# Performance work log

Measured on AMD Instinct MI355X. Metric: run time of the kernel, lower is better.

Reference implementation:

```python
import jax, jax.numpy as jnp
import numpy as np

N = 4096
IN_F = 256
OUT_F = 64
HEADS = 8
ALPHA = 0.2  # LeakyReLU negative slope


def setup_inputs() -> dict:
    key = jax.random.key(0)
    k1, k2, k3, k4 = jax.random.split(key, 4)
    X = jax.random.normal(k1, (N, IN_F), dtype=jnp.float32)
    adj = jax.random.randint(k2, (N, N), 0, 2, dtype=jnp.int32)
    # self-loops so every row has at least one neighbor (softmax well-defined)
    idx = jnp.arange(N)
    adj = adj.at[idx, idx].set(1)
    W = jax.random.normal(k3, (HEADS, IN_F, OUT_F), dtype=jnp.float32) * 0.05
    a = jax.random.normal(k4, (HEADS, 2 * OUT_F, 1), dtype=jnp.float32) * 0.05
    return {"X": X, "adj": adj, "W": W, "a": a}


def reference(X, adj, W, a):
    # H: [heads, N, F]
    H = jnp.einsum('ni,hio->hno', X, W)
    F_ = H.shape[-1]
    # cat([h_i, h_j]) @ a  ==  h_i @ a[:F] + h_j @ a[F:]
    a1 = a[:, :F_, 0]   # [heads, F]
    a2 = a[:, F_:, 0]   # [heads, F]
    f1 = jnp.einsum('hnf,hf->hn', H, a1)  # score contribution of row node i
    f2 = jnp.einsum('hnf,hf->hn', H, a2)  # score contribution of col node j
    e = jax.nn.leaky_relu(f1[:, :, None] + f2[:, None, :], negative_slope=ALPHA)  # [heads, N, N]
    e = jnp.where(adj[None, :, :] == 0, -jnp.inf, e)
    attention = jax.nn.softmax(e, axis=-1)
    # dropout omitted (eval mode)
    H_out = jnp.einsum('hnm,hmf->hnf', attention, H)  # [heads, N, F]
    return H_out.mean(axis=0)  # [N, F]
```

## Files before the change

kernel.cpp:

```cpp
#include <hip/hip_runtime.h>
#include <hip/hip_bf16.h>

#define N_NODES 4096
#define IN_F 256
#define OUT_F 64
#define HEADS 8
#define ALPHA 0.2f

typedef _Float16 f16x8 __attribute__((ext_vector_type(8)));
typedef float f32x4 __attribute__((ext_vector_type(4)));
union U4 { uint4 u; f16x8 h; unsigned w[4]; };

#define WFRAG_OFF 0
#define BFRAG_OFF (WFRAG_OFF + 8*8*4*64*8*2)
#define F1_OFF    (BFRAG_OFF + 8*128*4*64*8*2)
#define GP_OFF    (F1_OFF + 8*4096*4)
#define GN_OFF    (GP_OFF + 8*4096*2)
#define ADJ_OFF   (GN_OFF + 8*4096*2)

static __device__ __forceinline__ unsigned pkmul(unsigned a, unsigned b) {
  unsigned r; asm("v_pk_mul_f16 %0, %1, %2" : "=v"(r) : "v"(a), "v"(b)); return r;
}
static __device__ __forceinline__ unsigned pkmax(unsigned a, unsigned b) {
  unsigned r; asm("v_pk_max_f16 %0, %1, %2" : "=v"(r) : "v"(a), "v"(b)); return r;
}
static __device__ __forceinline__ unsigned short f2h_bits(float f) {
  return __builtin_bit_cast(unsigned short, (_Float16)f);
}

__global__ __launch_bounds__(256) void k_misc(
    const int* __restrict__ adj, const float* __restrict__ W,
    unsigned long long* __restrict__ bits, _Float16* __restrict__ wfrag,
    float* __restrict__ out) {
  int b = blockIdx.x, t = threadIdx.x;
  if (b < 2048) {
    int lane = t & 63;
    int waveid = b * 4 + (t >> 6);
    for (int it = 0; it < 32; ++it) {
      int widx = waveid + it * 8192;
      int v = adj[(size_t)widx * 64 + lane];
      unsigned long long m = __ballot(v != 0);
      if (lane == 0) bits[widx] = m;
    }
  } else {
    int h = b - 2048;
    for (int pos = t; pos < 2048; pos += 256) {
      int kt = pos >> 8, ct = (pos >> 6) & 3, l = pos & 63;
      int lr = l & 15, lg = l >> 4;
#pragma unroll
      for (int e = 0; e < 8; ++e)
        wfrag[(size_t)(((h*8 + kt)*4 + ct)*64 + l) * 8 + e]
          = (_Float16)W[(size_t)(h*256 + kt*32 + lg*8 + e) * 64 + ct*16 + lr];
    }
    float4* oz = ((float4*)out) + h * 8192;
    float4 zz = make_float4(0.f, 0.f, 0.f, 0.f);
    for (int q = t; q < 8192; q += 256) oz[q] = zz;
  }
}

__global__ __launch_bounds__(256) void k_hf(
    const float* __restrict__ X, const _Float16* __restrict__ wfrag,
    const float* __restrict__ a, _Float16* __restrict__ bfrag,
    float* __restrict__ f1, _Float16* __restrict__ Gp, _Float16* __restrict__ Gn) {
  int b = blockIdx.x, t = threadIdx.x;
  int h = b & 7, rb = b >> 3;
  int w = t >> 6, l = t & 63;
  int i0 = rb * 64 + w * 16;
  int r = l & 15, g = l >> 4;
  const U4* wv = (const U4*)wfrag;
  f32x4 z = {0.f, 0.f, 0.f, 0.f};
  f32x4 acc[4] = {z, z, z, z};
#pragma unroll
  for (int kt = 0; kt < 8; ++kt) {
    const float4* xr = (const float4*)(X + (size_t)(i0 + r) * 256 + (kt*4 + g) * 8);
    float4 x0 = xr[0], x1 = xr[1];
    U4 af;
    af.h[0] = (_Float16)x0.x; af.h[1] = (_Float16)x0.y;
    af.h[2] = (_Float16)x0.z; af.h[3] = (_Float16)x0.w;
    af.h[4] = (_Float16)x1.x; af.h[5] = (_Float16)x1.y;
    af.h[6] = (_Float16)x1.z; af.h[7] = (_Float16)x1.w;
#pragma unroll
    for (int ct = 0; ct < 4; ++ct) {
      U4 bv = wv[((h*8 + kt)*4 + ct)*64 + l];
      acc[ct] = __builtin_amdgcn_mfma_f32_16x16x32_f16(af.h, bv.h, acc[ct], 0, 0, 0);
    }
  }
  int jb = i0 + g*4;
#pragma unroll
  for (int ct = 0; ct < 4; ++ct) {
    size_t base = ((((size_t)h*128 + (jb>>5))*4 + ct)*64 + ((jb>>3)&3)*16 + r) * 8
                  + (jb & 7);
    union { short4 s; _Float16 hh[4]; } sv;
#pragma unroll
    for (int ri = 0; ri < 4; ++ri) sv.hh[ri] = (_Float16)acc[ct][ri];
    *(short4*)(bfrag + base) = sv.s;
  }
  float a1v[4], a2v[4];
#pragma unroll
  for (int ct = 0; ct < 4; ++ct) {
    a1v[ct] = a[h*128 + ct*16 + r];
    a2v[ct] = a[h*128 + 64 + ct*16 + r];
  }
#pragma unroll
  for (int ri = 0; ri < 4; ++ri) {
    float s1 = acc[0][ri]*a1v[0] + acc[1][ri]*a1v[1]
             + acc[2][ri]*a1v[2] + acc[3][ri]*a1v[3];
    float s2 = acc[0][ri]*a2v[0] + acc[1][ri]*a2v[1]
             + acc[2][ri]*a2v[2] + acc[3][ri]*a2v[3];
#pragma unroll
    for (int off = 1; off < 16; off <<= 1) {
      s1 += __shfl_xor(s1, off);
      s2 += __shfl_xor(s2, off);
    }
    if (r == 0) {
      int row = i0 + g*4 + ri;
      f1[h*4096 + row] = s1;
      Gp[h*4096 + row] = (_Float16)__expf(s2);
      Gn[h*4096 + row] = (_Float16)__expf(ALPHA * s2);
    }
  }
}

#define ATTN_BODY(PF, JT, DOPF) {                                              \
  U4 gp, gn;                                                                   \
  gp.u = Gs[0][(JT)*4 + g].u;                                                  \
  gn.u = Gs[1][(JT)*4 + g].u;                                                  \
  U4 b0, b1, b2, b3;                                                           \
  b0.u = PF[0]; b1.u = PF[1]; b2.u = PF[2]; b3.u = PF[3];                      \
  _Pragma("unroll")                                                            \
  for (int rg = 0; rg < 4; ++rg) {                                             \
    unsigned wm = Lb[rg*16 + r][JT];                                           \
    U4 av;                                                                     \
    _Pragma("unroll")                                                          \
    for (int p = 0; p < 4; ++p) {                                              \
      unsigned pm = pkmax(pkmul(Epp[rg], gp.w[p]), pkmul(Enn[rg], gn.w[p]));   \
      av.w[p] = pm & MLUT[(wm >> (g8 + 2*p)) & 3u];                            \
    }                                                                          \
    acc[rg][0] = __builtin_amdgcn_mfma_f32_16x16x32_f16(av.h, b0.h, acc[rg][0], 0,0,0); \
    acc[rg][1] = __builtin_amdgcn_mfma_f32_16x16x32_f16(av.h, b1.h, acc[rg][1], 0,0,0); \
    acc[rg][2] = __builtin_amdgcn_mfma_f32_16x16x32_f16(av.h, b2.h, acc[rg][2], 0,0,0); \
    acc[rg][3] = __builtin_amdgcn_mfma_f32_16x16x32_f16(av.h, b3.h, acc[rg][3], 0,0,0); \
    dn[rg]     = __builtin_amdgcn_mfma_f32_16x16x32_f16(av.h, bones.h, dn[rg], 0,0,0);  \
  }                                                                            \
  if (DOPF) {                                                                  \
    _Pragma("unroll")                                                          \
    for (int c = 0; c < 4; ++c) PF[c] = bfh[((JT) + 2)*256 + c*64];            \
  }                                                                            \
}

#define WRBUF(buf) {                                                           \
  _Pragma("unroll")                                                            \
  for (int rg = 0; rg < 4; ++rg) {                                             \
    _Pragma("unroll")                                                          \
    for (int ct = 0; ct < 4; ++ct) buf[rg*4 + ct][l] = acc[rg][ct];            \
    buf[16 + rg][l] = dn[rg];                                                  \
  } }
#define ADBUF(buf) {                                                           \
  _Pragma("unroll")                                                            \
  for (int rg = 0; rg < 4; ++rg) {                                             \
    _Pragma("unroll")                                                          \
    for (int ct = 0; ct < 4; ++ct) acc[rg][ct] += buf[rg*4 + ct][l];           \
    dn[rg] += buf[16 + rg][l];                                                 \
  } }

__global__ __launch_bounds__(512) void k_attn(
    const float* __restrict__ f1, const unsigned int* __restrict__ adjbits,
    const _Float16* __restrict__ Gp, const _Float16* __restrict__ Gn,
    const _Float16* __restrict__ bfrag, float* __restrict__ out) {
  __shared__ __align__(16) char smem[49408];
  __shared__ unsigned MLUT[4];
  unsigned (*Lb)[129] = (unsigned(*)[129])smem;
  U4 (*Gs)[512] = (U4(*)[512])(smem + 33024);
  f32x4 (*red0)[64] = (f32x4(*)[64])smem;
  f32x4 (*red1)[64] = (f32x4(*)[64])(smem + 20480);
  int b = blockIdx.x;
  int h = b & 7, rs = b >> 3;
  int i0 = rs * 64;
  int t = threadIdx.x, jq = t >> 6, l = t & 63;
  int r = l & 15, g = l >> 4, g8 = g * 8;
  if (t < 4) MLUT[t] = ((t & 1) ? 0xFFFFu : 0u) | ((t & 2) ? 0xFFFF0000u : 0u);
  for (int q = t; q < 8192; q += 512)
    Lb[q >> 7][q & 127] = adjbits[(size_t)(i0 + (q >> 7)) * 128 + (q & 127)];
  Gs[0][t].u = ((const uint4*)(Gp + (size_t)h * 4096))[t];
  Gs[1][t].u = ((const uint4*)(Gn + (size_t)h * 4096))[t];
  unsigned Epp[4], Enn[4];
#pragma unroll
  for (int rg = 0; rg < 4; ++rg) {
    float f1r = f1[h * N_NODES + i0 + rg*16 + r];
    unsigned short ep = f2h_bits(__expf(f1r));
    unsigned short en = f2h_bits(__expf(ALPHA * f1r));
    Epp[rg] = ep | ((unsigned)ep << 16);
    Enn[rg] = en | ((unsigned)en << 16);
  }
  unsigned ov = (r == 0) ? 0x3C003C00u : 0u;
  U4 bones; bones.u = make_uint4(ov, ov, ov, ov);
  const uint4* bfh = (const uint4*)bfrag + (size_t)h * 32768 + l;
  int jt0 = jq * 16;
  uint4 pA[4], pB[4];
#pragma unroll
  for (int c = 0; c < 4; ++c) pA[c] = bfh[jt0 * 256 + c*64];
#pragma unroll
  for (int c = 0; c < 4; ++c) pB[c] = bfh[(jt0 + 1) * 256 + c*64];
  __syncthreads();
  f32x4 z = {0.f,0.f,0.f,0.f};
  f32x4 acc[4][4] = {{z,z,z,z},{z,z,z,z},{z,z,z,z},{z,z,z,z}};
  f32x4 dn[4] = {z,z,z,z};
  for (int q2 = 0; q2 < 8; ++q2) {
    ATTN_BODY(pA, jt0 + q2*2,     (q2 < 7));
    ATTN_BODY(pB, jt0 + q2*2 + 1, (q2 < 7));
  }
  __syncthreads();
  if (jq == 1) WRBUF(red0);
  if (jq == 5) WRBUF(red1);
  __syncthreads();
  if (jq == 0) ADBUF(red0);
  if (jq == 4) ADBUF(red1);
  __syncthreads();
  if (jq == 3) WRBUF(red0);
  if (jq == 7) WRBUF(red1);
  __syncthreads();
  if (jq == 2) ADBUF(red0);
  if (jq == 6) ADBUF(red1);
  __syncthreads();
  if (jq == 2) WRBUF(red0);
  if (jq == 6) WRBUF(red1);
  __syncthreads();
  if (jq == 0) ADBUF(red0);
  if (jq == 4) ADBUF(red1);
  __syncthreads();
  if (jq == 4) WRBUF(red0);
  __syncthreads();
  if (jq == 0) {
    ADBUF(red0);
#pragma unroll
    for (int rg = 0; rg < 4; ++rg)
#pragma unroll
      for (int ri = 0; ri < 4; ++ri) {
        float den = __shfl(dn[rg][ri], l & 48);
        float sc = 0.125f / den;
        float* op = out + (size_t)(i0 + rg*16 + g*4 + ri) * 64;
        atomicAdd(op + r,      acc[rg][0][ri] * sc);
        atomicAdd(op + 16 + r, acc[rg][1][ri] * sc);
        atomicAdd(op + 32 + r, acc[rg][2][ri] * sc);
        atomicAdd(op + 48 + r, acc[rg][3][ri] * sc);
      }
  }
}

extern "C" void kernel_launch(void* const* d_in, const int* in_sizes, int n_in,
                              void* d_out, int out_size, void* d_ws, size_t ws_size,
                              hipStream_t stream) {
  const float* X = (const float*)d_in[0];
  const int* adj = (const int*)d_in[1];
  const float* W = (const float*)d_in[2];
  const float* a = (const float*)d_in[3];
  float* out = (float*)d_out;
  char* ws = (char*)d_ws;

  _Float16* wfrag = (_Float16*)(ws + WFRAG_OFF);
  _Float16* bfrag = (_Float16*)(ws + BFRAG_OFF);
  float* f1 = (float*)(ws + F1_OFF);
  _Float16* Gp = (_Float16*)(ws + GP_OFF);
  _Float16* Gn = (_Float16*)(ws + GN_OFF);
  unsigned long long* bits64 = (unsigned long long*)(ws + ADJ_OFF);
  const unsigned int* bits32 = (const unsigned int*)(ws + ADJ_OFF);

  k_misc<<<dim3(2056), dim3(256), 0, stream>>>(adj, W, bits64, wfrag, out);
  k_hf<<<dim3(512), dim3(256), 0, stream>>>(X, wfrag, a, bfrag, f1, Gp, Gn);
  k_attn<<<dim3(512), dim3(512), 0, stream>>>(f1, bits32, Gp, Gn, bfrag, out);
}
```

Measured before the change: 79.24 us.

## Fuse prep kernels, repartition attention waves, compute denominators with packed adds

```diff
diff --git a/kernel.cpp b/kernel.cpp
--- a/kernel.cpp
+++ b/kernel.cpp
@@ -11,8 +11,7 @@
 typedef float f32x4 __attribute__((ext_vector_type(4)));
 union U4 { uint4 u; f16x8 h; unsigned w[4]; };
 
-#define WFRAG_OFF 0
-#define BFRAG_OFF (WFRAG_OFF + 8*8*4*64*8*2)
+#define BFRAG_OFF 0
 #define F1_OFF    (BFRAG_OFF + 8*128*4*64*8*2)
 #define GP_OFF    (F1_OFF + 8*4096*4)
 #define GN_OFF    (GP_OFF + 8*4096*2)
@@ -24,14 +23,23 @@
 static __device__ __forceinline__ unsigned pkmax(unsigned a, unsigned b) {
   unsigned r; asm("v_pk_max_f16 %0, %1, %2" : "=v"(r) : "v"(a), "v"(b)); return r;
 }
+static __device__ __forceinline__ unsigned pkadd(unsigned a, unsigned b) {
+  unsigned r; asm("v_pk_add_f16 %0, %1, %2" : "=v"(r) : "v"(a), "v"(b)); return r;
+}
 static __device__ __forceinline__ unsigned short f2h_bits(float f) {
   return __builtin_bit_cast(unsigned short, (_Float16)f);
 }
-
-__global__ __launch_bounds__(256) void k_misc(
-    const int* __restrict__ adj, const float* __restrict__ W,
-    unsigned long long* __restrict__ bits, _Float16* __restrict__ wfrag,
+static __device__ __forceinline__ float h2f(unsigned short x) {
+  return (float)__builtin_bit_cast(_Float16, x);
+}
+
+__global__ __launch_bounds__(256) void k_all(
+    const float* __restrict__ X, const int* __restrict__ adj,
+    const float* __restrict__ W, const float* __restrict__ a,
+    unsigned long long* __restrict__ bits, _Float16* __restrict__ bfrag,
+    float* __restrict__ f1, _Float16* __restrict__ Gp, _Float16* __restrict__ Gn,
     float* __restrict__ out) {
+  __shared__ _Float16 wf[16384];
   int b = blockIdx.x, t = threadIdx.x;
   if (b < 2048) {
     int lane = t & 63;
@@ -42,32 +50,22 @@
       unsigned long long m = __ballot(v != 0);
       if (lane == 0) bits[widx] = m;
     }
-  } else {
-    int h = b - 2048;
-    for (int pos = t; pos < 2048; pos += 256) {
-      int kt = pos >> 8, ct = (pos >> 6) & 3, l = pos & 63;
-      int lr = l & 15, lg = l >> 4;
-#pragma unroll
-      for (int e = 0; e < 8; ++e)
-        wfrag[(size_t)(((h*8 + kt)*4 + ct)*64 + l) * 8 + e]
-          = (_Float16)W[(size_t)(h*256 + kt*32 + lg*8 + e) * 64 + ct*16 + lr];
-    }
-    float4* oz = ((float4*)out) + h * 8192;
-    float4 zz = make_float4(0.f, 0.f, 0.f, 0.f);
-    for (int q = t; q < 8192; q += 256) oz[q] = zz;
-  }
-}
-
-__global__ __launch_bounds__(256) void k_hf(
-    const float* __restrict__ X, const _Float16* __restrict__ wfrag,
-    const float* __restrict__ a, _Float16* __restrict__ bfrag,
-    float* __restrict__ f1, _Float16* __restrict__ Gp, _Float16* __restrict__ Gn) {
-  int b = blockIdx.x, t = threadIdx.x;
-  int h = b & 7, rb = b >> 3;
+    return;
+  }
+  int b2 = b - 2048;
+  int h = b2 >> 6, rb = b2 & 63;
+  const float* Wh = W + (size_t)h * 16384;
+  for (int q = t; q < 16384; q += 256) {
+    float wv = Wh[q];
+    int k = q >> 6, f = q & 63;
+    int kt = k >> 5, lg = (k >> 3) & 3, e = k & 7;
+    int ct = f >> 4, lr = f & 15;
+    wf[(size_t)(((kt*4 + ct)*64) + lg*16 + lr) * 8 + e] = (_Float16)wv;
+  }
+  __syncthreads();
   int w = t >> 6, l = t & 63;
   int i0 = rb * 64 + w * 16;
   int r = l & 15, g = l >> 4;
-  const U4* wv = (const U4*)wfrag;
   f32x4 z = {0.f, 0.f, 0.f, 0.f};
   f32x4 acc[4] = {z, z, z, z};
 #pragma unroll
@@ -81,7 +79,7 @@
     af.h[6] = (_Float16)x1.z; af.h[7] = (_Float16)x1.w;
 #pragma unroll
     for (int ct = 0; ct < 4; ++ct) {
-      U4 bv = wv[((h*8 + kt)*4 + ct)*64 + l];
+      U4 bv = *(const U4*)(wf + (size_t)(((kt*4 + ct)*64) + l) * 8);
       acc[ct] = __builtin_amdgcn_mfma_f32_16x16x32_f16(af.h, bv.h, acc[ct], 0, 0, 0);
     }
   }
@@ -119,17 +117,22 @@
       Gn[h*4096 + row] = (_Float16)__expf(ALPHA * s2);
     }
   }
+  if (h == 0) {
+    float4* oz = (float4*)(out + (size_t)(rb * 64) * 64);
+    float4 zz = make_float4(0.f, 0.f, 0.f, 0.f);
+    for (int q = t; q < 1024; q += 256) oz[q] = zz;
+  }
 }
 
 #define ATTN_BODY(PF, JT, DOPF) {                                              \
   U4 gp, gn;                                                                   \
-  gp.u = Gs[0][(JT)*4 + g].u;                                                  \
-  gn.u = Gs[1][(JT)*4 + g].u;                                                  \
+  gp.u = Gs0[(JT)*4 + g].u;                                                    \
+  gn.u = Gs1[(JT)*4 + g].u;                                                    \
   U4 b0, b1, b2, b3;                                                           \
   b0.u = PF[0]; b1.u = PF[1]; b2.u = PF[2]; b3.u = PF[3];                      \
   _Pragma("unroll")                                                            \
-  for (int rg = 0; rg < 4; ++rg) {                                             \
-    unsigned wm = Lb[rg*16 + r][JT];                                           \
+  for (int rg = 0; rg < 2; ++rg) {                                             \
+    unsigned wm = Lb[rh32 + rg*16 + r][JT];                                    \
     U4 av;                                                                     \
     _Pragma("unroll")                                                          \
     for (int p = 0; p < 4; ++p) {                                              \
@@ -140,7 +143,9 @@
     acc[rg][1] = __builtin_amdgcn_mfma_f32_16x16x32_f16(av.h, b1.h, acc[rg][1], 0,0,0); \
     acc[rg][2] = __builtin_amdgcn_mfma_f32_16x16x32_f16(av.h, b2.h, acc[rg][2], 0,0,0); \
     acc[rg][3] = __builtin_amdgcn_mfma_f32_16x16x32_f16(av.h, b3.h, acc[rg][3], 0,0,0); \
-    dn[rg]     = __builtin_amdgcn_mfma_f32_16x16x32_f16(av.h, bones.h, dn[rg], 0,0,0);  \
+    unsigned sden = pkadd(pkadd(av.w[0], av.w[1]), pkadd(av.w[2], av.w[3]));   \
+    den[rg] += h2f((unsigned short)(sden & 0xFFFFu))                           \
+             + h2f((unsigned short)(sden >> 16));                              \
   }                                                                            \
   if (DOPF) {                                                                  \
     _Pragma("unroll")                                                          \
@@ -148,97 +153,91 @@
   }                                                                            \
 }
 
-#define WRBUF(buf) {                                                           \
+#define WRBUF(i) {                                                             \
   _Pragma("unroll")                                                            \
-  for (int rg = 0; rg < 4; ++rg) {                                             \
-    _Pragma("unroll")                                                          \
-    for (int ct = 0; ct < 4; ++ct) buf[rg*4 + ct][l] = acc[rg][ct];            \
-    buf[16 + rg][l] = dn[rg];                                                  \
-  } }
-#define ADBUF(buf) {                                                           \
+  for (int rg = 0; rg < 2; ++rg)                                               \
+    _Pragma("unroll")                                                          \
+    for (int ct = 0; ct < 4; ++ct) redp[(i)*576 + (rg*4+ct)*64 + l] = acc[rg][ct]; \
+  f32x4 dv = {den[0], den[1], 0.f, 0.f};                                       \
+  redp[(i)*576 + 512 + l] = dv;                                                \
+}
+#define ADBUF(i) {                                                             \
   _Pragma("unroll")                                                            \
-  for (int rg = 0; rg < 4; ++rg) {                                             \
-    _Pragma("unroll")                                                          \
-    for (int ct = 0; ct < 4; ++ct) acc[rg][ct] += buf[rg*4 + ct][l];           \
-    dn[rg] += buf[16 + rg][l];                                                 \
-  } }
-
-__global__ __launch_bounds__(512) void k_attn(
+  for (int rg = 0; rg < 2; ++rg)                                               \
+    _Pragma("unroll")                                                          \
+    for (int ct = 0; ct < 4; ++ct) acc[rg][ct] += redp[(i)*576 + (rg*4+ct)*64 + l]; \
+  f32x4 dv = redp[(i)*576 + 512 + l];                                          \
+  den[0] += dv[0]; den[1] += dv[1];                                            \
+}
+
+__global__ __launch_bounds__(512, 4) void k_attn(
     const float* __restrict__ f1, const unsigned int* __restrict__ adjbits,
     const _Float16* __restrict__ Gp, const _Float16* __restrict__ Gn,
     const _Float16* __restrict__ bfrag, float* __restrict__ out) {
   __shared__ __align__(16) char smem[49408];
   __shared__ unsigned MLUT[4];
   unsigned (*Lb)[129] = (unsigned(*)[129])smem;
-  U4 (*Gs)[512] = (U4(*)[512])(smem + 33024);
-  f32x4 (*red0)[64] = (f32x4(*)[64])smem;
-  f32x4 (*red1)[64] = (f32x4(*)[64])(smem + 20480);
+  U4* Gs0 = (U4*)(smem + 33024);
+  U4* Gs1 = (U4*)(smem + 41216);
+  f32x4* redp = (f32x4*)smem;
   int b = blockIdx.x;
   int h = b & 7, rs = b >> 3;
   int i0 = rs * 64;
-  int t = threadIdx.x, jq = t >> 6, l = t & 63;
+  int t = threadIdx.x, wid = t >> 6, l = t & 63;
+  int rh = wid >> 2, jq = wid & 3;
+  int rh32 = rh * 32;
   int r = l & 15, g = l >> 4, g8 = g * 8;
   if (t < 4) MLUT[t] = ((t & 1) ? 0xFFFFu : 0u) | ((t & 2) ? 0xFFFF0000u : 0u);
+  const uint4* bfh = (const uint4*)bfrag + (size_t)h * 32768 + l;
+  int jt0 = jq * 32;
+  uint4 pA[4], pB[4];
+#pragma unroll
+  for (int c = 0; c < 4; ++c) pA[c] = bfh[jt0 * 256 + c*64];
+#pragma unroll
+  for (int c = 0; c < 4; ++c) pB[c] = bfh[(jt0 + 1) * 256 + c*64];
   for (int q = t; q < 8192; q += 512)
     Lb[q >> 7][q & 127] = adjbits[(size_t)(i0 + (q >> 7)) * 128 + (q & 127)];
-  Gs[0][t].u = ((const uint4*)(Gp + (size_t)h * 4096))[t];
-  Gs[1][t].u = ((const uint4*)(Gn + (size_t)h * 4096))[t];
-  unsigned Epp[4], Enn[4];
-#pragma unroll
-  for (int rg = 0; rg < 4; ++rg) {
-    float f1r = f1[h * N_NODES + i0 + rg*16 + r];
+  Gs0[t].u = ((const uint4*)(Gp + (size_t)h * 4096))[t];
+  Gs1[t].u = ((const uint4*)(Gn + (size_t)h * 4096))[t];
+  unsigned Epp[2], Enn[2];
+#pragma unroll
+  for (int rg = 0; rg < 2; ++rg) {
+    float f1r = f1[h * N_NODES + i0 + rh32 + rg*16 + r];
     unsigned short ep = f2h_bits(__expf(f1r));
     unsigned short en = f2h_bits(__expf(ALPHA * f1r));
     Epp[rg] = ep | ((unsigned)ep << 16);
     Enn[rg] = en | ((unsigned)en << 16);
   }
-  unsigned ov = (r == 0) ? 0x3C003C00u : 0u;
-  U4 bones; bones.u = make_uint4(ov, ov, ov, ov);
-  const uint4* bfh = (const uint4*)bfrag + (size_t)h * 32768 + l;
-  int jt0 = jq * 16;
-  uint4 pA[4], pB[4];
-#pragma unroll
-  for (int c = 0; c < 4; ++c) pA[c] = bfh[jt0 * 256 + c*64];
-#pragma unroll
-  for (int c = 0; c < 4; ++c) pB[c] = bfh[(jt0 + 1) * 256 + c*64];
   __syncthreads();
   f32x4 z = {0.f,0.f,0.f,0.f};
-  f32x4 acc[4][4] = {{z,z,z,z},{z,z,z,z},{z,z,z,z},{z,z,z,z}};
-  f32x4 dn[4] = {z,z,z,z};
-  for (int q2 = 0; q2 < 8; ++q2) {
-    ATTN_BODY(pA, jt0 + q2*2,     (q2 < 7));
-    ATTN_BODY(pB, jt0 + q2*2 + 1, (q2 < 7));
-  }
-  __syncthreads();
-  if (jq == 1) WRBUF(red0);
-  if (jq == 5) WRBUF(red1);
-  __syncthreads();
-  if (jq == 0) ADBUF(red0);
-  if (jq == 4) ADBUF(red1);
-  __syncthreads();
-  if (jq == 3) WRBUF(red0);
-  if (jq == 7) WRBUF(red1);
-  __syncthreads();
-  if (jq == 2) ADBUF(red0);
-  if (jq == 6) ADBUF(red1);
-  __syncthreads();
-  if (jq == 2) WRBUF(red0);
-  if (jq == 6) WRBUF(red1);
-  __syncthreads();
-  if (jq == 0) ADBUF(red0);
-  if (jq == 4) ADBUF(red1);
-  __syncthreads();
-  if (jq == 4) WRBUF(red0);
+  f32x4 acc[2][4] = {{z,z,z,z},{z,z,z,z}};
+  float den[2] = {0.f, 0.f};
+  for (int q2 = 0; q2 < 16; ++q2) {
+    ATTN_BODY(pA, jt0 + q2*2,     (q2 < 15));
+    ATTN_BODY(pB, jt0 + q2*2 + 1, (q2 < 15));
+  }
+  __syncthreads();
+  if (jq == 1 || jq == 3) WRBUF(rh*2 + (jq >> 1));
+  __syncthreads();
+  if (jq == 0) ADBUF(rh*2);
+  if (jq == 2) ADBUF(rh*2 + 1);
+  __syncthreads();
+  if (jq == 2) WRBUF(rh);
   __syncthreads();
   if (jq == 0) {
-    ADBUF(red0);
-#pragma unroll
-    for (int rg = 0; rg < 4; ++rg)
+    ADBUF(rh);
+#pragma unroll
+    for (int rg = 0; rg < 2; ++rg) {
+      den[rg] += __shfl_xor(den[rg], 16);
+      den[rg] += __shfl_xor(den[rg], 32);
+    }
+#pragma unroll
+    for (int rg = 0; rg < 2; ++rg)
 #pragma unroll
       for (int ri = 0; ri < 4; ++ri) {
-        float den = __shfl(dn[rg][ri], l & 48);
-        float sc = 0.125f / den;
-        float* op = out + (size_t)(i0 + rg*16 + g*4 + ri) * 64;
+        float dr = __shfl(den[rg], g*4 + ri);
+        float sc = 0.125f / dr;
+        float* op = out + (size_t)(i0 + rh32 + rg*16 + g*4 + ri) * 64;
         atomicAdd(op + r,      acc[rg][0][ri] * sc);
         atomicAdd(op + 16 + r, acc[rg][1][ri] * sc);
         atomicAdd(op + 32 + r, acc[rg][2][ri] * sc);
@@ -257,7 +256,6 @@
   float* out = (float*)d_out;
   char* ws = (char*)d_ws;
 
-  _Float16* wfrag = (_Float16*)(ws + WFRAG_OFF);
   _Float16* bfrag = (_Float16*)(ws + BFRAG_OFF);
   float* f1 = (float*)(ws + F1_OFF);
   _Float16* Gp = (_Float16*)(ws + GP_OFF);
@@ -265,7 +263,7 @@
   unsigned long long* bits64 = (unsigned long long*)(ws + ADJ_OFF);
   const unsigned int* bits32 = (const unsigned int*)(ws + ADJ_OFF);
 
-  k_misc<<<dim3(2056), dim3(256), 0, stream>>>(adj, W, bits64, wfrag, out);
-  k_hf<<<dim3(512), dim3(256), 0, stream>>>(X, wfrag, a, bfrag, f1, Gp, Gn);
+  k_all<<<dim3(2560), dim3(256), 0, stream>>>(X, adj, W, a, bits64, bfrag,
+                                              f1, Gp, Gn, out);
   k_attn<<<dim3(512), dim3(512), 0, stream>>>(f1, bits32, Gp, Gn, bfrag, out);
 }
```

Result: no change. 77.78 us (-1.8%).
